# Performance work log

Hardware: AMD Instinct MI355X
Metric: run time of the kernel (lower is better)

The kernel has to match this reference:

```python
import jax, jax.numpy as jnp
import numpy as np

NEG = -1e30   # finite stand-in for -inf (keeps vjp NaN-free)
BLANK = 0


def _ctc_loss_mean(logits, targets):
    """CTC loss matching torch.nn.CTCLoss(blank=0, zero_infinity=True,
    reduction='mean') applied to log_softmax(logits).permute(1,0,2), with
    input_lengths = T and uniform target_lengths = L.

    logits:  (B, T, K) raw scores
    targets: (B, L) int labels in [1, K) (no blanks)
    """
    B, T, K = logits.shape
    L = targets.shape[1]
    S = 2 * L + 1  # extended label sequence: blank-interleaved

    logp = jax.nn.log_softmax(logits, axis=-1)  # (B, T, K)

    # extended labels ext = [blank, y1, blank, y2, ..., yL, blank]
    ext = jnp.full((B, S), BLANK, dtype=targets.dtype)
    ext = ext.at[:, 1::2].set(targets)  # (B, S)

    # per-step log-probs of extended labels: lp[b, t, s] = logp[b, t, ext[b, s]]
    lp = jnp.take_along_axis(logp, ext[:, None, :], axis=2)  # (B, T, S)

    # skip transition (s-2 -> s) allowed iff ext[s] != blank and ext[s] != ext[s-2]
    skip = jnp.concatenate(
        [jnp.zeros((B, 2), dtype=bool),
         (ext[:, 2:] != BLANK) & (ext[:, 2:] != ext[:, :-2])], axis=1)  # (B, S)

    # alpha init at t = 0
    alpha0 = jnp.full((B, S), NEG, dtype=logp.dtype)
    alpha0 = alpha0.at[:, 0].set(lp[:, 0, 0]).at[:, 1].set(lp[:, 0, 1])

    pad1 = jnp.full((B, 1), NEG, dtype=logp.dtype)
    pad2 = jnp.full((B, 2), NEG, dtype=logp.dtype)

    def step(alpha, lp_t):
        a1 = alpha                                            # stay
        a2 = jnp.concatenate([pad1, alpha[:, :-1]], axis=1)   # advance 1
        a3 = jnp.concatenate([pad2, alpha[:, :-2]], axis=1)   # advance 2
        a3 = jnp.where(skip, a3, NEG)
        new = jnp.logaddexp(jnp.logaddexp(a1, a2), a3) + lp_t
        return new, None

    xs = jnp.swapaxes(lp[:, 1:, :], 0, 1)  # (T-1, B, S)
    alpha, _ = jax.lax.scan(step, alpha0, xs)

    # total log-likelihood: end at last blank or last label
    logl = jnp.logaddexp(alpha[:, S - 1], alpha[:, S - 2])  # (B,)

    per = -logl / L  # 'mean' reduction divides each loss by target length
    per = jnp.where(logl > -1e29, per, 0.0)  # zero_infinity
    return jnp.mean(per)


def setup_inputs() -> dict:
    key = jax.random.key(0)
    k1, k2 = jax.random.split(key)
    B, T, K, L = 64, 1024, 512, 100
    logits = jax.random.normal(k1, (B, T, K), dtype=jnp.float32)
    targets = jax.random.randint(k2, (B, L), 1, K)  # labels exclude blank=0
    return {"logits": logits, "targets": targets}


def reference(logits, targets):
    return _ctc_loss_mean(logits, targets)
```

## Files before the change

kernel.cpp:

```cpp
#include <hip/hip_runtime.h>
#include <hip/hip_fp16.h>


#define TT 1024
#define BB 64
#define KK 512
#define LL 100

static constexpr float L2E = 1.44269504088896340736f;
static constexpr float LN2 = 0.69314718055994530942f;

__device__ __forceinline__ float dpp_shr1_z(float x) {
  return __builtin_bit_cast(float,
      __builtin_amdgcn_update_dpp(0, __builtin_bit_cast(int, x),
                                  0x138, 0xf, 0xf, true));
}
__device__ __forceinline__ int dpp_shr1_zi(int x) {
  return __builtin_amdgcn_update_dpp(0, x, 0x138, 0xf, 0xf, true);
}
__device__ __forceinline__ float slog2(float x) {
  return x > 0.0f ? log2f(x) : -1.0e30f;
}
__device__ __forceinline__ float2 upk(unsigned u) {
  return __half22float2(__builtin_bit_cast(__half2, u));
}

__device__ __forceinline__ float wave_max_dpp(float v) {
#define DPPMAX(C)                                                          \
  v = fmaxf(v, __builtin_bit_cast(float, __builtin_amdgcn_update_dpp(      \
                   0, __builtin_bit_cast(int, v), C, 0xf, 0xf, true)))
  DPPMAX(0x111); DPPMAX(0x112); DPPMAX(0x114); DPPMAX(0x118);
  DPPMAX(0x142); DPPMAX(0x143);
#undef DPPMAX
  return __builtin_bit_cast(float,
      __builtin_amdgcn_readlane(__builtin_bit_cast(int, v), 63));
}
__device__ __forceinline__ float wave_sum_dpp(float v) {
#define DPPADD(C)                                                          \
  v = v + __builtin_bit_cast(float, __builtin_amdgcn_update_dpp(           \
              0, __builtin_bit_cast(int, v), C, 0xf, 0xf, true))
  DPPADD(0x111); DPPADD(0x112); DPPADD(0x114); DPPADD(0x118);
  DPPADD(0x142); DPPADD(0x143);
#undef DPPADD
  return __builtin_bit_cast(float,
      __builtin_amdgcn_readlane(__builtin_bit_cast(int, v), 63));
}

__device__ __forceinline__ void resc(float& S0, float& S1, float& S2,
                                     float& S3, int& ea, float& f1,
                                     float& f2) {
  const float m = fmaxf(fmaxf(S0, S1), fmaxf(S2, S3));
  int E = (int)((__float_as_uint(m) >> 23) & 255) - 127;
  E = (m > 0.0f) ? E : 0;
  const float sc = __uint_as_float((unsigned)(127 - E) << 23);
  S0 *= sc; S1 *= sc; S2 *= sc; S3 *= sc;
  ea += E;
  int dE = dpp_shr1_zi(ea) - ea;
  dE = dE < -250 ? -250 : (dE > 250 ? 250 : dE);
  const int h = dE / 2;
  f1 = __uint_as_float((unsigned)(127 + h) << 23);
  f2 = __uint_as_float((unsigned)(127 + (dE - h)) << 23);
}
__device__ __forceinline__ void refresh_f(int ea, float& f1, float& f2) {
  int dE = dpp_shr1_zi(ea) - ea;
  dE = dE < -250 ? -250 : (dE > 250 ? 250 : dE);
  const int h = dE / 2;
  f1 = __uint_as_float((unsigned)(127 + h) << 23);
  f2 = __uint_as_float((unsigned)(127 + (dE - h)) << 23);
}

__device__ __forceinline__ void fstep(float2 r, float mA, float mB,
                                      float& S0, float& S1, float& S2,
                                      float& S3, float f1, float f2) {
  const float A3 = dpp_shr1_z(S3) * f1 * f2;
  const float n0 = S0 + A3;
  const float n1 = (S0 + S1 + mA * A3) * r.x;
  const float n2 = S1 + S2;
  const float n3 = (S2 + S3 + mB * S1) * r.y;
  S0 = n0; S1 = n1; S2 = n2; S3 = n3;
}
__device__ __forceinline__ void bstep(float2 r, float mBb, float mAn,
                                      float& S0, float& S1, float& S2,
                                      float& S3, float f1, float f2) {
  const float s2 = dpp_shr1_z(r.x);
  const float H0 = dpp_shr1_z(S0) * f1 * f2;
  const float H1 = dpp_shr1_z(S1) * f1 * f2;
  const float u = r.x * S1;
  const float v = r.y * S3;
  const float n0 = S0 + u;
  const float n1 = u + fmaf(mBb, v, S2);
  const float n2 = S2 + v;
  const float n3 = v + fmaf(mAn, s2 * H1, H0);
  S0 = n0; S1 = n1; S2 = n2; S3 = n3;
}

template <int CB, int NC>
__device__ __forceinline__ void run_fwd(const unsigned* __restrict__ gb,
                                        float mA, float mB, float& S0,
                                        float& S1, float& S2, float& S3,
                                        int& ea, float& f1, float& f2) {
  uint2 RA[8], RB[8], RC[8], RD[8];
#define ISSUE(BUF, CHN)                                                    \
  do {                                                                     \
    if ((CHN) < NC) {                                                      \
      _Pragma("unroll") for (int j = 0; j < 8; ++j)                        \
        BUF[j] = *reinterpret_cast<const uint2*>(                          \
            gb + (size_t)((CB + (CHN)) * 8 + j) * 128);                    \
      __builtin_amdgcn_sched_barrier(0);                                   \
    }                                                                      \
  } while (0)
#define COMP(BUF)                                                          \
  do {                                                                     \
    _Pragma("unroll") for (int j = 0; j < 8; ++j) {                        \
      fstep(upk(BUF[j].x), mA, mB, S0, S1, S2, S3, f1, f2);                \
      fstep(upk(BUF[j].y), mA, mB, S0, S1, S2, S3, f1, f2);                \
      if ((j & 3) == 3) resc(S0, S1, S2, S3, ea, f1, f2);                  \
    }                                                                      \
  } while (0)
  ISSUE(RA, 0); ISSUE(RB, 1); ISSUE(RC, 2);
  for (int c = 0; c < NC; c += 4) {
    ISSUE(RD, c + 3); COMP(RA);
    ISSUE(RA, c + 4); COMP(RB);
    ISSUE(RB, c + 5); COMP(RC);
    ISSUE(RC, c + 6); COMP(RD);
  }
#undef ISSUE
#undef COMP
}

template <int CB, int NC>
__device__ __forceinline__ void run_bwd(const unsigned* __restrict__ gb,
                                        float mBb, float mAn, float& S0,
                                        float& S1, float& S2, float& S3,
                                        int& ea, float& f1, float& f2) {
  uint2 RA[8], RB[8], RC[8], RD[8];
#define ISSUE(BUF, CHN)                                                    \
  do {                                                                     \
    if ((CHN) < NC) {                                                      \
      _Pragma("unroll") for (int j = 0; j < 8; ++j)                        \
        BUF[j] = *reinterpret_cast<const uint2*>(                          \
            gb + (size_t)(511 - ((CB + (CHN)) * 8 + j)) * 128);            \
      __builtin_amdgcn_sched_barrier(0);                                   \
    }                                                                      \
  } while (0)
#define COMP(BUF)                                                          \
  do {                                                                     \
    _Pragma("unroll") for (int j = 0; j < 8; ++j) {                        \
      bstep(upk(BUF[j].y), mBb, mAn, S0, S1, S2, S3, f1, f2);              \
      bstep(upk(BUF[j].x), mBb, mAn, S0, S1, S2, S3, f1, f2);              \
      if ((j & 3) == 3) resc(S0, S1, S2, S3, ea, f1, f2);                  \
    }                                                                      \
  } while (0)
  ISSUE(RA, 0); ISSUE(RB, 1); ISSUE(RC, 2);
  for (int c = 0; c < NC; c += 4) {
    ISSUE(RD, c + 3); COMP(RA);
    ISSUE(RA, c + 4); COMP(RB);
    ISSUE(RB, c + 5); COMP(RC);
    ISSUE(RC, c + 6); COMP(RD);
  }
#undef ISSUE
#undef COMP
}

__device__ __forceinline__ void prob_row(const float* __restrict__ logits,
                                         const int* __restrict__ targets,
                                         unsigned* __restrict__ pk,
                                         float* __restrict__ lbArr,
                                         int b, int t, int lane, float* sp) {
  const int row = (b << 10) + t;
  const float* x = logits + (size_t)row * KK;
  const float4 v0 = reinterpret_cast<const float4*>(x)[lane];
  const float4 v1 = reinterpret_cast<const float4*>(x)[lane + 64];
  float4* sp4 = reinterpret_cast<float4*>(sp);
  sp4[lane] = v0;
  sp4[lane + 64] = v1;

  float m = fmaxf(fmaxf(fmaxf(v0.x, v0.y), fmaxf(v0.z, v0.w)),
                  fmaxf(fmaxf(v1.x, v1.y), fmaxf(v1.z, v1.w)));
  m = wave_max_dpp(m);

  float e = exp2f((v0.x - m) * L2E) + exp2f((v0.y - m) * L2E) +
            exp2f((v0.z - m) * L2E) + exp2f((v0.w - m) * L2E) +
            exp2f((v1.x - m) * L2E) + exp2f((v1.y - m) * L2E) +
            exp2f((v1.z - m) * L2E) + exp2f((v1.w - m) * L2E);
  e = wave_sum_dpp(e);

  __syncthreads();
  const float xb = sp[0];

  float ox = 0.0f, oy = 0.0f;
  if (lane >= 1 && lane <= 50) {
    const int2 c = *reinterpret_cast<const int2*>(
        targets + b * LL + (2 * lane - 2));
    ox = exp2f((sp[c.x] - xb) * L2E);
    oy = exp2f((sp[c.y] - xb) * L2E);
  }
  const int word = (lane == 0) ? 63 : (lane - 1);
  const __half2 h = __floats2half2_rn(ox, oy);
  pk[(size_t)(row >> 1) * 128 + word * 2 + (row & 1)] =
      __builtin_bit_cast(unsigned, h);
  if (lane == 0) lbArr[row] = (xb - m) * L2E + 9.0f - log2f(e);
}

__device__ __forceinline__ void fwd_masks(const int* tg, int lane,
                                          float& mA, float& mB) {
  mA = 0.0f; mB = 0.0f;
  if (lane > 0 && 2 * lane <= LL - 1)
    mA = (tg[2 * lane] != tg[2 * lane - 1]) ? 1.0f : 0.0f;
  if (2 * lane + 1 <= LL - 1)
    mB = (tg[2 * lane + 1] != tg[2 * lane]) ? 1.0f : 0.0f;
}
__device__ __forceinline__ void bwd_masks(const int* tg, int lane,
                                          float& mBb, float& mAn, int& w) {
  const int ii = 50 - lane;
  w = (ii >= 0) ? ii : 50;
  mBb = 0.0f; mAn = 0.0f;
  if (ii >= 0 && 2 * ii + 1 <= LL - 1)
    mBb = (tg[2 * ii + 1] != tg[2 * ii]) ? 1.0f : 0.0f;
  if (ii >= 0 && ii <= 48)
    mAn = (tg[2 * ii + 2] != tg[2 * ii + 1]) ? 1.0f : 0.0f;
}

__global__ __launch_bounds__(256) void k_p1(
    const float* __restrict__ logits, const int* __restrict__ targets,
    unsigned* __restrict__ pk, float* __restrict__ lbArr,
    float* __restrict__ out) {
  if (blockIdx.x == 0 && threadIdx.x == 0) out[0] = 0.0f;
  const int wv = threadIdx.x >> 6;
  const int lane = threadIdx.x & 63;
  __shared__ float sx[4][KK];
  const int e = (blockIdx.x << 2) + wv;
  const int b = e / 384;
  const int w = e - b * 384;
  const int t = (w < 192) ? w : (w + 640);
  prob_row(logits, targets, pk, lbArr, b, t, lane, sx[wv]);
}

__global__ __launch_bounds__(256) void k_mid1(
    const float* __restrict__ logits, const int* __restrict__ targets,
    unsigned* __restrict__ pk, float* __restrict__ lbArr,
    float* __restrict__ st1) {
  const int lane = threadIdx.x & 63;
  const int wv = threadIdx.x >> 6;
  __shared__ float sx[4][KK];

  if (blockIdx.x >= BB) {
    const int e = ((blockIdx.x - BB) << 2) + wv;
    const int b = e / 384;
    const int w = e - b * 384;
    const int t = (w < 192) ? (w + 192) : (w + 448);
    prob_row(logits, targets, pk, lbArr, b, t, lane, sx[wv]);
    return;
  }
  if (wv >= 2) return;
  const int b = blockIdx.x;
  const int dir = wv;
  const int* tg = targets + b * LL;

  float S0 = 0.0f, S1 = 0.0f, S2 = 0.0f, S3 = 0.0f;
  int ea = 0;
  float f1 = 1.0f, f2 = 1.0f;

  if (dir == 0) {
    const unsigned* gb = pk + (size_t)b * 512 * 128 + lane * 2;
    float mA, mB;
    fwd_masks(tg, lane, mA, mB);
    S0 = (lane == 0) ? 1.0f : 0.0f;
    run_fwd<0, 12>(gb, mA, mB, S0, S1, S2, S3, ea, f1, f2);
  } else {
    float mBb, mAn; int w;
    bwd_masks(tg, lane, mBb, mAn, w);
    const unsigned* gb = pk + (size_t)b * 512 * 128 + w * 2;
    if (lane == 0) S0 = 1.0f;
    if (lane == 1) S3 = 1.0f;
    run_bwd<0, 12>(gb, mBb, mAn, S0, S1, S2, S3, ea, f1, f2);
  }
  float* stp = st1 + (size_t)(b * 2 + dir) * 5 * 64;
  stp[0 * 64 + lane] = S0;
  stp[1 * 64 + lane] = S1;
  stp[2 * 64 + lane] = S2;
  stp[3 * 64 + lane] = S3;
  stp[4 * 64 + lane] = __int_as_float(ea);
}

__global__ __launch_bounds__(256) void k_mid2(
    const float* __restrict__ logits, const int* __restrict__ targets,
    unsigned* __restrict__ pk, float* __restrict__ lbArr,
    const float* __restrict__ st1, float* __restrict__ st2) {
  const int lane = threadIdx.x & 63;
  const int wv = threadIdx.x >> 6;
  __shared__ float sx[4][KK];

  if (blockIdx.x >= BB) {
    const int e = ((blockIdx.x - BB) << 2) + wv;
    const int b = e >> 8;
    const int w = e & 255;
    prob_row(logits, targets, pk, lbArr, b, 384 + w, lane, sx[wv]);
    return;
  }
  if (wv >= 2) return;
  const int b = blockIdx.x;
  const int dir = wv;
  const int* tg = targets + b * LL;

  const float* sp = st1 + (size_t)(b * 2 + dir) * 5 * 64;
  float S0 = sp[0 * 64 + lane];
  float S1 = sp[1 * 64 + lane];
  float S2 = sp[2 * 64 + lane];
  float S3 = sp[3 * 64 + lane];
  int ea = __float_as_int(sp[4 * 64 + lane]);
  float f1, f2;
  refresh_f(ea, f1, f2);

  if (dir == 0) {
    const unsigned* gb = pk + (size_t)b * 512 * 128 + lane * 2;
    float mA, mB;
    fwd_masks(tg, lane, mA, mB);
    run_fwd<12, 12>(gb, mA, mB, S0, S1, S2, S3, ea, f1, f2);
  } else {
    float mBb, mAn; int w;
    bwd_masks(tg, lane, mBb, mAn, w);
    const unsigned* gb = pk + (size_t)b * 512 * 128 + w * 2;
    run_bwd<12, 12>(gb, mBb, mAn, S0, S1, S2, S3, ea, f1, f2);
  }
  float* stp = st2 + (size_t)(b * 2 + dir) * 5 * 64;
  stp[0 * 64 + lane] = S0;
  stp[1 * 64 + lane] = S1;
  stp[2 * 64 + lane] = S2;
  stp[3 * 64 + lane] = S3;
  stp[4 * 64 + lane] = __int_as_float(ea);
}

__global__ __launch_bounds__(128) void k_tail(
    const unsigned* __restrict__ pk, const float* __restrict__ lbArr,
    const int* __restrict__ targets, const float* __restrict__ st2,
    float* __restrict__ out) {
  const int lane = threadIdx.x & 63;
  const int wv = threadIdx.x >> 6;
  const int b = blockIdx.x;
  const int dir = wv;
  const int* tg = targets + b * LL;

  __shared__ float sG[6][64];

  const float4* lbv = reinterpret_cast<const float4*>(lbArr + (size_t)b * TT);
  const int lbbase = (dir == 0) ? 0 : 128;
  const float4 lb0 = lbv[lbbase + lane];
  const float4 lb1 = lbv[lbbase + lane + 64];

  const float* sp = st2 + (size_t)(b * 2 + dir) * 5 * 64;
  float S0 = sp[0 * 64 + lane];
  float S1 = sp[1 * 64 + lane];
  float S2 = sp[2 * 64 + lane];
  float S3 = sp[3 * 64 + lane];
  int ea = __float_as_int(sp[4 * 64 + lane]);
  float f1, f2;
  refresh_f(ea, f1, f2);

  if (dir == 0) {
    const unsigned* gb = pk + (size_t)b * 512 * 128 + lane * 2;
    float mA, mB;
    fwd_masks(tg, lane, mA, mB);
    run_fwd<24, 8>(gb, mA, mB, S0, S1, S2, S3, ea, f1, f2);
  } else {
    float mBb, mAn; int w;
    bwd_masks(tg, lane, mBb, mAn, w);
    const unsigned* gb = pk + (size_t)b * 512 * 128 + w * 2;
    run_bwd<24, 8>(gb, mBb, mAn, S0, S1, S2, S3, ea, f1, f2);
  }

  float s4 = (lb0.x + lb0.y) + (lb0.z + lb0.w) +
             (lb1.x + lb1.y) + (lb1.z + lb1.w);
  #pragma unroll
  for (int d = 1; d < 64; d <<= 1) s4 += __shfl_xor(s4, d);

  if (dir == 1) {
    sG[0][lane] = S0; sG[1][lane] = S1; sG[2][lane] = S2; sG[3][lane] = S3;
    sG[4][lane] = (float)ea;
    if (lane == 0) sG[5][0] = s4;
  }
  __syncthreads();

  if (dir == 0) {
    const int gj = (lane <= 50) ? (50 - lane) : 63;
    const float eb = sG[4][gj];
    const float eff = (float)ea;
    float w0 = slog2(S0) + eff + slog2(sG[0][gj]) + eb;
    float w1 = slog2(S1) + eff + slog2(sG[1][gj]) + eb;
    float w2 = slog2(S2) + eff + slog2(sG[2][gj]) + eb;
    float w3 = slog2(S3) + eff + slog2(sG[3][gj]) + eb;
    float wm = fmaxf(fmaxf(w0, w1), fmaxf(w2, w3));
    #pragma unroll
    for (int d = 1; d < 64; d <<= 1) wm = fmaxf(wm, __shfl_xor(wm, d));
    float ss = exp2f(w0 - wm) + exp2f(w1 - wm) +
               exp2f(w2 - wm) + exp2f(w3 - wm);
    #pragma unroll
    for (int d = 1; d < 64; d <<= 1) ss += __shfl_xor(ss, d);

    if (lane == 0) {
      const float lbsum = s4 + sG[5][0];
      float loss = 0.0f;
      if (wm > -1.0e29f) {
        const float logl2 = wm + log2f(ss) + lbsum - (float)(TT * 9);
        loss = -(logl2 * LN2) / (float)LL;
      }
      atomicAdd(out, loss * (1.0f / (float)BB));
    }
  }
}

extern "C" void kernel_launch(void* const* d_in, const int* in_sizes, int n_in,
                              void* d_out, int out_size, void* d_ws, size_t ws_size,
                              hipStream_t stream) {
  const float* logits = (const float*)d_in[0];
  const int* targets = (const int*)d_in[1];
  float* out = (float*)d_out;

  unsigned* pk = (unsigned*)d_ws;
  float* lbArr = (float*)d_ws + (size_t)BB * 512 * 128;
  float* st1 = lbArr + (size_t)BB * TT;
  float* st2 = st1 + (size_t)BB * 2 * 5 * 64;

  hipLaunchKernelGGL(k_p1, dim3(BB * 384 / 4), dim3(256), 0, stream,
                     logits, targets, pk, lbArr, out);
  hipLaunchKernelGGL(k_mid1, dim3(BB + BB * 384 / 4), dim3(256), 0, stream,
                     logits, targets, pk, lbArr, st1);
  hipLaunchKernelGGL(k_mid2, dim3(BB + BB * 256 / 4), dim3(256), 0, stream,
                     logits, targets, pk, lbArr, st1, st2);
  hipLaunchKernelGGL(k_tail, dim3(BB), dim3(128), 0, stream,
                     pk, lbArr, targets, st2, out);
}
```

Before: 48.46 us.

## Merge mid stages into one kernel and rebalance prob rows across launches

Collapses the four-kernel pipeline into three. The first kernel now computes 640 edge time rows per batch. A single middle kernel runs 20 recurrence chunks while it computes the remaining 384 center rows, and the tail kernel finishes with 12 chunks. It also reads the blank logit with a wave readlane instead of a block-wide barrier plus a shared-memory read. This removes one launch and one state round-trip, but the center-row production has to stay ahead of the longer recurrence.

```diff
diff --git a/kernel.cpp b/kernel.cpp
--- a/kernel.cpp
+++ b/kernel.cpp
@@ -185,8 +185,8 @@
             exp2f((v1.z - m) * L2E) + exp2f((v1.w - m) * L2E);
   e = wave_sum_dpp(e);
 
-  __syncthreads();
-  const float xb = sp[0];
+  const float xb = __builtin_bit_cast(float,
+      __builtin_amdgcn_readlane(__builtin_bit_cast(int, v0.x), 0));
 
   float ox = 0.0f, oy = 0.0f;
   if (lane >= 1 && lane <= 50) {
@@ -221,7 +221,7 @@
     mAn = (tg[2 * ii + 2] != tg[2 * ii + 1]) ? 1.0f : 0.0f;
 }
 
-__global__ __launch_bounds__(256) void k_p1(
+__global__ __launch_bounds__(256) void k_probs_edge(
     const float* __restrict__ logits, const int* __restrict__ targets,
     unsigned* __restrict__ pk, float* __restrict__ lbArr,
     float* __restrict__ out) {
@@ -230,16 +230,16 @@
   const int lane = threadIdx.x & 63;
   __shared__ float sx[4][KK];
   const int e = (blockIdx.x << 2) + wv;
-  const int b = e / 384;
-  const int w = e - b * 384;
-  const int t = (w < 192) ? w : (w + 640);
+  const int b = e / 640;
+  const int w = e - b * 640;
+  const int t = (w < 320) ? w : (w + 384);
   prob_row(logits, targets, pk, lbArr, b, t, lane, sx[wv]);
 }
 
-__global__ __launch_bounds__(256) void k_mid1(
+__global__ __launch_bounds__(256) void k_mid(
     const float* __restrict__ logits, const int* __restrict__ targets,
     unsigned* __restrict__ pk, float* __restrict__ lbArr,
-    float* __restrict__ st1) {
+    float* __restrict__ st) {
   const int lane = threadIdx.x & 63;
   const int wv = threadIdx.x >> 6;
   __shared__ float sx[4][KK];
@@ -248,8 +248,7 @@
     const int e = ((blockIdx.x - BB) << 2) + wv;
     const int b = e / 384;
     const int w = e - b * 384;
-    const int t = (w < 192) ? (w + 192) : (w + 448);
-    prob_row(logits, targets, pk, lbArr, b, t, lane, sx[wv]);
+    prob_row(logits, targets, pk, lbArr, b, 320 + w, lane, sx[wv]);
     return;
   }
   if (wv >= 2) return;
@@ -266,16 +265,16 @@
     float mA, mB;
     fwd_masks(tg, lane, mA, mB);
     S0 = (lane == 0) ? 1.0f : 0.0f;
-    run_fwd<0, 12>(gb, mA, mB, S0, S1, S2, S3, ea, f1, f2);
+    run_fwd<0, 20>(gb, mA, mB, S0, S1, S2, S3, ea, f1, f2);
   } else {
     float mBb, mAn; int w;
     bwd_masks(tg, lane, mBb, mAn, w);
     const unsigned* gb = pk + (size_t)b * 512 * 128 + w * 2;
     if (lane == 0) S0 = 1.0f;
     if (lane == 1) S3 = 1.0f;
-    run_bwd<0, 12>(gb, mBb, mAn, S0, S1, S2, S3, ea, f1, f2);
-  }
-  float* stp = st1 + (size_t)(b * 2 + dir) * 5 * 64;
+    run_bwd<0, 20>(gb, mBb, mAn, S0, S1, S2, S3, ea, f1, f2);
+  }
+  float* stp = st + (size_t)(b * 2 + dir) * 5 * 64;
   stp[0 * 64 + lane] = S0;
   stp[1 * 64 + lane] = S1;
   stp[2 * 64 + lane] = S2;
@@ -283,27 +282,24 @@
   stp[4 * 64 + lane] = __int_as_float(ea);
 }
 
-__global__ __launch_bounds__(256) void k_mid2(
-    const float* __restrict__ logits, const int* __restrict__ targets,
-    unsigned* __restrict__ pk, float* __restrict__ lbArr,
-    const float* __restrict__ st1, float* __restrict__ st2) {
+__global__ __launch_bounds__(128) void k_tail(
+    const unsigned* __restrict__ pk, const float* __restrict__ lbArr,
+    const int* __restrict__ targets, const float* __restrict__ st,
+    float* __restrict__ out) {
   const int lane = threadIdx.x & 63;
   const int wv = threadIdx.x >> 6;
-  __shared__ float sx[4][KK];
-
-  if (blockIdx.x >= BB) {
-    const int e = ((blockIdx.x - BB) << 2) + wv;
-    const int b = e >> 8;
-    const int w = e & 255;
-    prob_row(logits, targets, pk, lbArr, b, 384 + w, lane, sx[wv]);
-    return;
-  }
-  if (wv >= 2) return;
   const int b = blockIdx.x;
   const int dir = wv;
   const int* tg = targets + b * LL;
 
-  const float* sp = st1 + (size_t)(b * 2 + dir) * 5 * 64;
+  __shared__ float sG[6][64];
+
+  const float4* lbv = reinterpret_cast<const float4*>(lbArr + (size_t)b * TT);
+  const int lbbase = (dir == 0) ? 0 : 128;
+  const float4 lb0 = lbv[lbbase + lane];
+  const float4 lb1 = lbv[lbbase + lane + 64];
+
+  const float* sp = st + (size_t)(b * 2 + dir) * 5 * 64;
   float S0 = sp[0 * 64 + lane];
   float S1 = sp[1 * 64 + lane];
   float S2 = sp[2 * 64 + lane];
@@ -316,57 +312,12 @@
     const unsigned* gb = pk + (size_t)b * 512 * 128 + lane * 2;
     float mA, mB;
     fwd_masks(tg, lane, mA, mB);
-    run_fwd<12, 12>(gb, mA, mB, S0, S1, S2, S3, ea, f1, f2);
+    run_fwd<20, 12>(gb, mA, mB, S0, S1, S2, S3, ea, f1, f2);
   } else {
     float mBb, mAn; int w;
     bwd_masks(tg, lane, mBb, mAn, w);
     const unsigned* gb = pk + (size_t)b * 512 * 128 + w * 2;
-    run_bwd<12, 12>(gb, mBb, mAn, S0, S1, S2, S3, ea, f1, f2);
-  }
-  float* stp = st2 + (size_t)(b * 2 + dir) * 5 * 64;
-  stp[0 * 64 + lane] = S0;
-  stp[1 * 64 + lane] = S1;
-  stp[2 * 64 + lane] = S2;
-  stp[3 * 64 + lane] = S3;
-  stp[4 * 64 + lane] = __int_as_float(ea);
-}
-
-__global__ __launch_bounds__(128) void k_tail(
-    const unsigned* __restrict__ pk, const float* __restrict__ lbArr,
-    const int* __restrict__ targets, const float* __restrict__ st2,
-    float* __restrict__ out) {
-  const int lane = threadIdx.x & 63;
-  const int wv = threadIdx.x >> 6;
-  const int b = blockIdx.x;
-  const int dir = wv;
-  const int* tg = targets + b * LL;
-
-  __shared__ float sG[6][64];
-
-  const float4* lbv = reinterpret_cast<const float4*>(lbArr + (size_t)b * TT);
-  const int lbbase = (dir == 0) ? 0 : 128;
-  const float4 lb0 = lbv[lbbase + lane];
-  const float4 lb1 = lbv[lbbase + lane + 64];
-
-  const float* sp = st2 + (size_t)(b * 2 + dir) * 5 * 64;
-  float S0 = sp[0 * 64 + lane];
-  float S1 = sp[1 * 64 + lane];
-  float S2 = sp[2 * 64 + lane];
-  float S3 = sp[3 * 64 + lane];
-  int ea = __float_as_int(sp[4 * 64 + lane]);
-  float f1, f2;
-  refresh_f(ea, f1, f2);
-
-  if (dir == 0) {
-    const unsigned* gb = pk + (size_t)b * 512 * 128 + lane * 2;
-    float mA, mB;
-    fwd_masks(tg, lane, mA, mB);
-    run_fwd<24, 8>(gb, mA, mB, S0, S1, S2, S3, ea, f1, f2);
-  } else {
-    float mBb, mAn; int w;
-    bwd_masks(tg, lane, mBb, mAn, w);
-    const unsigned* gb = pk + (size_t)b * 512 * 128 + w * 2;
-    run_bwd<24, 8>(gb, mBb, mAn, S0, S1, S2, S3, ea, f1, f2);
+    run_bwd<20, 12>(gb, mBb, mAn, S0, S1, S2, S3, ea, f1, f2);
   }
 
   float s4 = (lb0.x + lb0.y) + (lb0.z + lb0.w) +
@@ -418,15 +369,12 @@
 
   unsigned* pk = (unsigned*)d_ws;
   float* lbArr = (float*)d_ws + (size_t)BB * 512 * 128;
-  float* st1 = lbArr + (size_t)BB * TT;
-  float* st2 = st1 + (size_t)BB * 2 * 5 * 64;
-
-  hipLaunchKernelGGL(k_p1, dim3(BB * 384 / 4), dim3(256), 0, stream,
+  float* st = lbArr + (size_t)BB * TT;
+
+  hipLaunchKernelGGL(k_probs_edge, dim3(BB * 640 / 4), dim3(256), 0, stream,
                      logits, targets, pk, lbArr, out);
-  hipLaunchKernelGGL(k_mid1, dim3(BB + BB * 384 / 4), dim3(256), 0, stream,
-                     logits, targets, pk, lbArr, st1);
-  hipLaunchKernelGGL(k_mid2, dim3(BB + BB * 256 / 4), dim3(256), 0, stream,
-                     logits, targets, pk, lbArr, st1, st2);
+  hipLaunchKernelGGL(k_mid, dim3(BB + BB * 384 / 4), dim3(256), 0, stream,
+                     logits, targets, pk, lbArr, st);
   hipLaunchKernelGGL(k_tail, dim3(BB), dim3(128), 0, stream,
-                     pk, lbArr, targets, st2, out);
-}
+                     pk, lbArr, targets, st, out);
+}
```

Measured after the change: 47.80 us. No clear change (-1.4%).
